# Optimization experiments

Measured on AMD Instinct MI355X. Metric: run time of the kernel, lower is better.

The kernel has to match this reference:

```python
import jax, jax.numpy as jnp
import numpy as np

N_SEND = 100000   # sender nodes
N_RECV = 100000   # receiver nodes
E = 600000        # edges
D = 128           # node feature channels (128x0e)
A = 8             # attr channels (8x0e)
S = 64            # edge scalar dim = fc_neurons[0]
H = 128           # fc hidden = fc_neurons[1]; tp.weight_numel = 128
NUM_NEIGHBORS = 32.0
SILU_NORM = 1.679177  # e3nn normalize2mom constant for silu: (E[silu(N(0,1))^2])^-0.5


def fctp(x, y, W):
    """e3nn FullyConnectedTensorProduct for all-scalar (0e) irreps:
    single 'uvw' path, path weight 1/sqrt(mul_u*mul_v)."""
    return jnp.einsum('nu,nv,uvw->nw', x, y, W) / np.sqrt(x.shape[1] * y.shape[1]).astype(np.float32)


def setup_inputs() -> dict:
    key = jax.random.key(0)
    ks = jax.random.split(key, 14)
    return {
        'sender_input': jax.random.normal(ks[0], (N_SEND, D), jnp.float32),
        'sender_attr': jax.random.normal(ks[1], (N_SEND, A), jnp.float32),
        'receiver_input': jax.random.normal(ks[2], (N_RECV, D), jnp.float32),
        'receiver_attr': jax.random.normal(ks[3], (N_RECV, A), jnp.float32),
        'edge_src': jax.random.randint(ks[4], (E,), 0, N_SEND, jnp.int32),
        'edge_dst': jax.random.randint(ks[5], (E,), 0, N_RECV, jnp.int32),
        'edge_attr': jax.random.normal(ks[6], (E, 1), jnp.float32),
        'edge_scalars': jax.random.normal(ks[7], (E, S), jnp.float32),
        # e3nn TP weights are initialized N(0,1)
        'W_sc': jax.random.normal(ks[8], (D, A, D), jnp.float32),
        'W_lin1': jax.random.normal(ks[9], (D, A, D), jnp.float32),
        'W_fc1': jax.random.normal(ks[10], (S, H), jnp.float32),
        'W_fc2': jax.random.normal(ks[11], (H, D), jnp.float32),
        'W_lin2': jax.random.normal(ks[12], (D, A, D), jnp.float32),
        'W_lin3': jax.random.normal(ks[13], (D, A, 1), jnp.float32),
    }


def reference(sender_input, sender_attr, receiver_input, receiver_attr,
              edge_src, edge_dst, edge_attr, edge_scalars,
              W_sc, W_lin1, W_fc1, W_fc2, W_lin2, W_lin3):
    # FullyConnectedNet([S, H, weight_numel], silu): act(x@W/sqrt(fan_in)), last layer linear
    h = SILU_NORM * jax.nn.silu(edge_scalars @ W_fc1 / np.sqrt(S).astype(np.float32))
    weight = h @ W_fc2 / np.sqrt(H).astype(np.float32)                     # [E, D] per-edge TP weights

    receiver_self_connection = fctp(receiver_input, receiver_attr, W_sc)   # [Nr, D]
    sender_features = fctp(sender_input, sender_attr, W_lin1)              # [Ns, D]

    # gather -> per-edge weighted ('uvu') tensor product with 1x0e edge_attr -> scatter-add
    edge_features = weight * sender_features[edge_src] * edge_attr         # [E, D]
    receiver_features = jax.ops.segment_sum(edge_features, edge_dst,
                                            num_segments=receiver_input.shape[0])
    receiver_features = receiver_features / np.sqrt(NUM_NEIGHBORS).astype(np.float32)

    receiver_conv_out = fctp(receiver_features, receiver_attr, W_lin2)     # [Nr, D]
    receiver_angle = 0.1 * fctp(receiver_features, receiver_attr, W_lin3)  # [Nr, 1]
    # sc.output_mask is all-ones for this irreps config, so sin gating applies to all channels
    return jnp.cos(receiver_angle) * receiver_self_connection + jnp.sin(receiver_angle) * receiver_conv_out
```

## Files before the change

### kernel.cpp

```cpp
#include <hip/hip_runtime.h>
#include <hip/hip_bf16.h>
#include <math.h>

#define NS 100000
#define NR 100000
#define NE 600000
#define SILU_NORM 1.679177f

typedef __attribute__((ext_vector_type(8))) short short8;
typedef __attribute__((ext_vector_type(4))) float f32x4;

static __device__ __forceinline__ short f2bf(float f) {
    return __builtin_bit_cast(short, __float2bfloat16(f));
}

#define GLDS16(g, l)                                                         \
    __builtin_amdgcn_global_load_lds(                                        \
        (const __attribute__((address_space(1))) unsigned int*)(const void*)(g), \
        (__attribute__((address_space(3))) unsigned int*)(void*)(l), 16, 0, 0)

__global__ void swz_kernel(const float* __restrict__ W,
                           __hip_bfloat16* __restrict__ out, int total)
{
    int idx = blockIdx.x * 256 + threadIdx.x;
    if (idx >= total) return;
    int s = idx >> 12, r = idx & 4095;
    int f = r >> 9;  r &= 511;
    int quad = r >> 7; r &= 127;
    int wl = r >> 3;
    int j = r & 7;
    int k = s * 32 + quad * 8 + j;
    int w = f * 16 + wl;
    out[idx] = __float2bfloat16(W[(size_t)k * 128 + w]);
}

__global__ __launch_bounds__(256) void fctp_mfma_kernel(
    const float* __restrict__ x, const float* __restrict__ y,
    const __hip_bfloat16* __restrict__ Wswz, float* __restrict__ out,
    float scale, int N)
{
    __shared__ __hip_bfloat16 Wb[8192];
    __shared__ float xs[128 * 8];

    const int tid = threadIdx.x;
    const int lane = tid & 63;
    const int wv = tid >> 6;
    const int quad = lane >> 4;
    const int wl = lane & 15;
    const int n0 = blockIdx.x * 128;

    float ya[2][8];
    #pragma unroll
    for (int mt = 0; mt < 2; ++mt) {
        int node = n0 + wv * 32 + mt * 16 + wl;
        if (node >= N) node = N - 1;
        const float4* yp = (const float4*)(y + (size_t)node * 8);
        float4 a = yp[0], b = yp[1];
        ya[mt][0] = a.x; ya[mt][1] = a.y; ya[mt][2] = a.z; ya[mt][3] = a.w;
        ya[mt][4] = b.x; ya[mt][5] = b.y; ya[mt][6] = b.z; ya[mt][7] = b.w;
    }

    f32x4 acc[2][8];
    #pragma unroll
    for (int mt = 0; mt < 2; ++mt)
        #pragma unroll
        for (int f = 0; f < 8; ++f)
            acc[mt][f] = (f32x4){0.f, 0.f, 0.f, 0.f};

    for (int cc = 0; cc < 16; ++cc) {
        __syncthreads();
        {
            const char* src = (const char*)(Wswz + (size_t)cc * 8192);
            #pragma unroll
            for (int i = 0; i < 4; ++i) {
                int off = (i * 256 + tid) * 16;
                GLDS16(src + off, (char*)Wb + off);
            }
            int nl = tid >> 1, c4 = (tid & 1) * 4;
            int node = n0 + nl;
            if (node >= N) node = N - 1;
            GLDS16(x + (size_t)node * 128 + cc * 8 + c4, (char*)xs + tid * 16);
        }
        __syncthreads();

        #pragma unroll
        for (int ks = 0; ks < 2; ++ks) {
            short8 bfr[8];
            #pragma unroll
            for (int f = 0; f < 8; ++f)
                bfr[f] = *(const short8*)((const short*)Wb +
                                          (size_t)ks * 4096 + (f * 64 + lane) * 8);
            #pragma unroll
            for (int mt = 0; mt < 2; ++mt) {
                float xv = xs[(wv * 32 + mt * 16 + wl) * 8 + ks * 4 + quad];
                short8 af;
                #pragma unroll
                for (int v = 0; v < 8; ++v) af[v] = f2bf(xv * ya[mt][v]);
                #pragma unroll
                for (int f = 0; f < 8; ++f)
                    acc[mt][f] = __builtin_amdgcn_mfma_f32_16x16x32_bf16(
                        af, bfr[f], acc[mt][f], 0, 0, 0);
            }
        }
    }

    #pragma unroll
    for (int mt = 0; mt < 2; ++mt) {
        #pragma unroll
        for (int r = 0; r < 4; ++r) {
            int node = n0 + wv * 32 + mt * 16 + quad * 4 + r;
            if (node < N) {
                #pragma unroll
                for (int f = 0; f < 8; ++f)
                    out[(size_t)node * 128 + f * 16 + wl] = acc[mt][f][r] * scale;
            }
        }
    }
}

__global__ __launch_bounds__(256) void edge_mfma_kernel(
    const int* __restrict__ esrc, const int* __restrict__ edst,
    const float* __restrict__ eattr, const float* __restrict__ escal,
    const __hip_bfloat16* __restrict__ W1swz,
    const __hip_bfloat16* __restrict__ W2swz,
    const float* __restrict__ sf, float* __restrict__ rfeat)
{
    __shared__ __hip_bfloat16 esA[8192];
    __shared__ __hip_bfloat16 Wb[16384];
    __shared__ __hip_bfloat16 hA[16384];

    const int tid = threadIdx.x;
    const int lane = tid & 63;
    const int wv = tid >> 6;
    const int quad = lane >> 4;
    const int wl = lane & 15;
    const int e0 = blockIdx.x * 128;

    #pragma unroll
    for (int i = 0; i < 4; ++i) {
        int c = i * 256 + tid;
        int l = c & 63, mtc = (c >> 6) & 7, s = c >> 9;
        int e = e0 + mtc * 16 + (l & 15);
        if (e >= NE) e = NE - 1;
        int kb = s * 32 + (l >> 4) * 8;
        const float4* p = (const float4*)(escal + (size_t)e * 64 + kb);
        float4 aa = p[0], bb = p[1];
        short8 v;
        v[0] = f2bf(aa.x); v[1] = f2bf(aa.y); v[2] = f2bf(aa.z); v[3] = f2bf(aa.w);
        v[4] = f2bf(bb.x); v[5] = f2bf(bb.y); v[6] = f2bf(bb.z); v[7] = f2bf(bb.w);
        *(short8*)((short*)esA + (size_t)c * 8) = v;
    }
    #pragma unroll
    for (int i = 0; i < 4; ++i) {
        int off = (i * 256 + tid) * 16;
        GLDS16((const char*)W1swz + off, (char*)Wb + off);
    }
    __syncthreads();

    f32x4 acc1[2][8];
    #pragma unroll
    for (int mt = 0; mt < 2; ++mt)
        #pragma unroll
        for (int f = 0; f < 8; ++f) acc1[mt][f] = (f32x4){0.f, 0.f, 0.f, 0.f};

    #pragma unroll
    for (int ks = 0; ks < 2; ++ks) {
        short8 bfr[8];
        #pragma unroll
        for (int f = 0; f < 8; ++f)
            bfr[f] = *(const short8*)((const short*)Wb +
                                      (size_t)ks * 4096 + (f * 64 + lane) * 8);
        #pragma unroll
        for (int mt = 0; mt < 2; ++mt) {
            int MT = wv * 2 + mt;
            short8 af = *(const short8*)((const short*)esA +
                                         ((size_t)(ks * 8 + MT) * 64 + lane) * 8);
            #pragma unroll
            for (int f = 0; f < 8; ++f)
                acc1[mt][f] = __builtin_amdgcn_mfma_f32_16x16x32_bf16(
                    af, bfr[f], acc1[mt][f], 0, 0, 0);
        }
    }

    #pragma unroll
    for (int mt = 0; mt < 2; ++mt) {
        int MT = wv * 2 + mt;
        #pragma unroll
        for (int f = 0; f < 8; ++f) {
            int s2 = f >> 1;
            int q2 = ((f & 1) * 2 + (wl >> 3)) & 3;
            int j2 = wl & 7;
            #pragma unroll
            for (int r = 0; r < 4; ++r) {
                float t = acc1[mt][f][r] * 0.125f;
                float h = SILU_NORM * t / (1.f + __expf(-t));
                int lpos = q2 * 16 + quad * 4 + r;
                ((short*)hA)[((size_t)(s2 * 8 + MT) * 64 + lpos) * 8 + j2] = f2bf(h);
            }
        }
    }
    __syncthreads();
    #pragma unroll
    for (int i = 0; i < 8; ++i) {
        int off = (i * 256 + tid) * 16;
        GLDS16((const char*)W2swz + off, (char*)Wb + off);
    }
    __syncthreads();

    f32x4 acc2[2][8];
    #pragma unroll
    for (int mt = 0; mt < 2; ++mt)
        #pragma unroll
        for (int f = 0; f < 8; ++f) acc2[mt][f] = (f32x4){0.f, 0.f, 0.f, 0.f};

    #pragma unroll
    for (int ks = 0; ks < 4; ++ks) {
        short8 bfr[8];
        #pragma unroll
        for (int f = 0; f < 8; ++f)
            bfr[f] = *(const short8*)((const short*)Wb +
                                      (size_t)ks * 4096 + (f * 64 + lane) * 8);
        #pragma unroll
        for (int mt = 0; mt < 2; ++mt) {
            int MT = wv * 2 + mt;
            short8 af = *(const short8*)((const short*)hA +
                                         ((size_t)(ks * 8 + MT) * 64 + lane) * 8);
            #pragma unroll
            for (int f = 0; f < 8; ++f)
                acc2[mt][f] = __builtin_amdgcn_mfma_f32_16x16x32_bf16(
                    af, bfr[f], acc2[mt][f], 0, 0, 0);
        }
    }

    const float s128 = 0.08838834764831845f;
    #pragma unroll
    for (int mt = 0; mt < 2; ++mt) {
        int MT = wv * 2 + mt;
        #pragma unroll
        for (int r = 0; r < 4; ++r) {
            int e = e0 + MT * 16 + quad * 4 + r;
            if (e < NE) {
                int src = esrc[e], dst = edst[e];
                float ea = eattr[e] * s128;
                #pragma unroll
                for (int f = 0; f < 8; ++f) {
                    float val = acc2[mt][f][r] * ea *
                                sf[(size_t)src * 128 + f * 16 + wl];
                    atomicAdd(&rfeat[(size_t)dst * 128 + f * 16 + wl], val);
                }
            }
        }
    }
}

__global__ __launch_bounds__(256) void angle_kernel(
    const float* __restrict__ rfeat, const float* __restrict__ rattr,
    const float* __restrict__ W3, float* __restrict__ angle)
{
    const int node = (int)((blockIdx.x * 256 + threadIdx.x) >> 6);
    const int lane = threadIdx.x & 63;
    float acc = 0.f;
    #pragma unroll
    for (int j = 0; j < 16; ++j) {
        int k = lane + 64 * j;
        int u = k >> 3, v = k & 7;
        acc += rfeat[(size_t)node * 128 + u] * rattr[(size_t)node * 8 + v] * W3[k];
    }
    #pragma unroll
    for (int off = 32; off; off >>= 1) acc += __shfl_down(acc, off);
    if (lane == 0) angle[node] = acc * 5.524271728019903e-4f;
}

__global__ __launch_bounds__(256) void combine_kernel(
    const float* __restrict__ conv, const float* __restrict__ rsc,
    const float* __restrict__ angle, float* __restrict__ out)
{
    int idx = blockIdx.x * 256 + threadIdx.x;
    float a = angle[idx >> 5];
    float ca = __cosf(a), sa = __sinf(a);
    float4 c = ((const float4*)conv)[idx];
    float4 s = ((const float4*)rsc)[idx];
    float4 o;
    o.x = ca * s.x + sa * c.x;
    o.y = ca * s.y + sa * c.y;
    o.z = ca * s.z + sa * c.z;
    o.w = ca * s.w + sa * c.w;
    ((float4*)out)[idx] = o;
}

extern "C" void kernel_launch(void* const* d_in, const int* in_sizes, int n_in,
                              void* d_out, int out_size, void* d_ws, size_t ws_size,
                              hipStream_t stream)
{
    const float* sender_input   = (const float*)d_in[0];
    const float* sender_attr    = (const float*)d_in[1];
    const float* receiver_input = (const float*)d_in[2];
    const float* receiver_attr  = (const float*)d_in[3];
    const int*   edge_src  = (const int*)d_in[4];
    const int*   edge_dst  = (const int*)d_in[5];
    const float* edge_attr = (const float*)d_in[6];
    const float* edge_scal = (const float*)d_in[7];
    const float* W_sc   = (const float*)d_in[8];
    const float* W_lin1 = (const float*)d_in[9];
    const float* W_fc1  = (const float*)d_in[10];
    const float* W_fc2  = (const float*)d_in[11];
    const float* W_lin2 = (const float*)d_in[12];
    const float* W_lin3 = (const float*)d_in[13];

    char* ws = (char*)d_ws;
    float* sf    = (float*)(ws);
    float* rfeat = (float*)(ws + 51200000);
    float* angle = (float*)(ws + 102400000);
    __hip_bfloat16* Wl1s = (__hip_bfloat16*)(ws + 102800000);
    __hip_bfloat16* Wscs = (__hip_bfloat16*)(ws + 103062144);
    __hip_bfloat16* Wl2s = (__hip_bfloat16*)(ws + 103324288);
    __hip_bfloat16* W1s  = (__hip_bfloat16*)(ws + 103586432);
    __hip_bfloat16* W2s  = (__hip_bfloat16*)(ws + 103602816);
    float* conv = sf;
    float* rsc  = rfeat;

    swz_kernel<<<512, 256, 0, stream>>>(W_lin1, Wl1s, 131072);
    swz_kernel<<<512, 256, 0, stream>>>(W_sc,   Wscs, 131072);
    swz_kernel<<<512, 256, 0, stream>>>(W_lin2, Wl2s, 131072);
    swz_kernel<<<32,  256, 0, stream>>>(W_fc1,  W1s,  8192);
    swz_kernel<<<64,  256, 0, stream>>>(W_fc2,  W2s,  16384);

    hipMemsetAsync(rfeat, 0, (size_t)NR * 128 * 4, stream);

    fctp_mfma_kernel<<<(NS + 127) / 128, 256, 0, stream>>>(
        sender_input, sender_attr, Wl1s, sf, 0.03125f, NS);
    edge_mfma_kernel<<<(NE + 127) / 128, 256, 0, stream>>>(
        edge_src, edge_dst, edge_attr, edge_scal, W1s, W2s, sf, rfeat);
    angle_kernel<<<NR / 4, 256, 0, stream>>>(rfeat, receiver_attr, W_lin3, angle);
    fctp_mfma_kernel<<<(NR + 127) / 128, 256, 0, stream>>>(
        rfeat, receiver_attr, Wl2s, conv, 0.005524271728019903f, NR);
    fctp_mfma_kernel<<<(NR + 127) / 128, 256, 0, stream>>>(
        receiver_input, receiver_attr, Wscs, rsc, 0.03125f, NR);
    combine_kernel<<<NR * 128 / 4 / 256, 256, 0, stream>>>(
        conv, rsc, angle, (float*)d_out);
}
```

Baseline: 817.8 us.

## Fuse lin2, angle and combine into one kernel; stream edge weights from global

Replaces the separate angle, lin2 FCTP and combine kernels with one conv_fuse_kernel. It computes the lin2 MFMA product, accumulates the lin3 angle from the same outer-product values, and writes the final cos/sin blend directly. This removes the conv and angle intermediate round-trips through global memory and two launches. The edge kernel also drops its LDS staging of W_fc1/W_fc2 and the scalar tile, reading the B fragments straight from global/L2 and A fragments into registers, with launch bounds set to 4 blocks. That cuts LDS use and barriers to raise occupancy, at the cost of repeated global weight loads per wave.

Result: faster. 747.7 us (-8.6%).

```diff
diff --git a/kernel.cpp b/kernel.cpp
--- a/kernel.cpp
+++ b/kernel.cpp
@@ -118,15 +118,13 @@
     }
 }
 
-__global__ __launch_bounds__(256) void edge_mfma_kernel(
+__global__ __launch_bounds__(256, 4) void edge_mfma_kernel(
     const int* __restrict__ esrc, const int* __restrict__ edst,
     const float* __restrict__ eattr, const float* __restrict__ escal,
     const __hip_bfloat16* __restrict__ W1swz,
     const __hip_bfloat16* __restrict__ W2swz,
     const float* __restrict__ sf, float* __restrict__ rfeat)
 {
-    __shared__ __hip_bfloat16 esA[8192];
-    __shared__ __hip_bfloat16 Wb[16384];
     __shared__ __hip_bfloat16 hA[16384];
 
     const int tid = threadIdx.x;
@@ -136,26 +134,20 @@
     const int wl = lane & 15;
     const int e0 = blockIdx.x * 128;
 
-    #pragma unroll
-    for (int i = 0; i < 4; ++i) {
-        int c = i * 256 + tid;
-        int l = c & 63, mtc = (c >> 6) & 7, s = c >> 9;
-        int e = e0 + mtc * 16 + (l & 15);
-        if (e >= NE) e = NE - 1;
-        int kb = s * 32 + (l >> 4) * 8;
-        const float4* p = (const float4*)(escal + (size_t)e * 64 + kb);
-        float4 aa = p[0], bb = p[1];
-        short8 v;
-        v[0] = f2bf(aa.x); v[1] = f2bf(aa.y); v[2] = f2bf(aa.z); v[3] = f2bf(aa.w);
-        v[4] = f2bf(bb.x); v[5] = f2bf(bb.y); v[6] = f2bf(bb.z); v[7] = f2bf(bb.w);
-        *(short8*)((short*)esA + (size_t)c * 8) = v;
-    }
-    #pragma unroll
-    for (int i = 0; i < 4; ++i) {
-        int off = (i * 256 + tid) * 16;
-        GLDS16((const char*)W1swz + off, (char*)Wb + off);
-    }
-    __syncthreads();
+    short8 af1[2][2];
+    #pragma unroll
+    for (int ks = 0; ks < 2; ++ks)
+        #pragma unroll
+        for (int mt = 0; mt < 2; ++mt) {
+            int e = e0 + (wv * 2 + mt) * 16 + wl;
+            if (e >= NE) e = NE - 1;
+            const float4* p = (const float4*)(escal + (size_t)e * 64 + ks * 32 + quad * 8);
+            float4 a = p[0], b = p[1];
+            short8 v;
+            v[0] = f2bf(a.x); v[1] = f2bf(a.y); v[2] = f2bf(a.z); v[3] = f2bf(a.w);
+            v[4] = f2bf(b.x); v[5] = f2bf(b.y); v[6] = f2bf(b.z); v[7] = f2bf(b.w);
+            af1[ks][mt] = v;
+        }
 
     f32x4 acc1[2][8];
     #pragma unroll
@@ -164,23 +156,16 @@
         for (int f = 0; f < 8; ++f) acc1[mt][f] = (f32x4){0.f, 0.f, 0.f, 0.f};
 
     #pragma unroll
-    for (int ks = 0; ks < 2; ++ks) {
-        short8 bfr[8];
-        #pragma unroll
-        for (int f = 0; f < 8; ++f)
-            bfr[f] = *(const short8*)((const short*)Wb +
-                                      (size_t)ks * 4096 + (f * 64 + lane) * 8);
-        #pragma unroll
-        for (int mt = 0; mt < 2; ++mt) {
-            int MT = wv * 2 + mt;
-            short8 af = *(const short8*)((const short*)esA +
-                                         ((size_t)(ks * 8 + MT) * 64 + lane) * 8);
-            #pragma unroll
-            for (int f = 0; f < 8; ++f)
-                acc1[mt][f] = __builtin_amdgcn_mfma_f32_16x16x32_bf16(
-                    af, bfr[f], acc1[mt][f], 0, 0, 0);
-        }
-    }
+    for (int ks = 0; ks < 2; ++ks)
+        #pragma unroll
+        for (int f = 0; f < 8; ++f) {
+            short8 bfr = *(const short8*)((const short*)W1swz +
+                                          (size_t)ks * 4096 + (f * 64 + lane) * 8);
+            acc1[0][f] = __builtin_amdgcn_mfma_f32_16x16x32_bf16(
+                af1[ks][0], bfr, acc1[0][f], 0, 0, 0);
+            acc1[1][f] = __builtin_amdgcn_mfma_f32_16x16x32_bf16(
+                af1[ks][1], bfr, acc1[1][f], 0, 0, 0);
+        }
 
     #pragma unroll
     for (int mt = 0; mt < 2; ++mt) {
@@ -200,12 +185,6 @@
         }
     }
     __syncthreads();
-    #pragma unroll
-    for (int i = 0; i < 8; ++i) {
-        int off = (i * 256 + tid) * 16;
-        GLDS16((const char*)W2swz + off, (char*)Wb + off);
-    }
-    __syncthreads();
 
     f32x4 acc2[2][8];
     #pragma unroll
@@ -215,20 +194,18 @@
 
     #pragma unroll
     for (int ks = 0; ks < 4; ++ks) {
-        short8 bfr[8];
-        #pragma unroll
-        for (int f = 0; f < 8; ++f)
-            bfr[f] = *(const short8*)((const short*)Wb +
-                                      (size_t)ks * 4096 + (f * 64 + lane) * 8);
-        #pragma unroll
-        for (int mt = 0; mt < 2; ++mt) {
-            int MT = wv * 2 + mt;
-            short8 af = *(const short8*)((const short*)hA +
-                                         ((size_t)(ks * 8 + MT) * 64 + lane) * 8);
-            #pragma unroll
-            for (int f = 0; f < 8; ++f)
-                acc2[mt][f] = __builtin_amdgcn_mfma_f32_16x16x32_bf16(
-                    af, bfr[f], acc2[mt][f], 0, 0, 0);
+        short8 afA = *(const short8*)((const short*)hA +
+                                      ((size_t)(ks * 8 + wv * 2 + 0) * 64 + lane) * 8);
+        short8 afB = *(const short8*)((const short*)hA +
+                                      ((size_t)(ks * 8 + wv * 2 + 1) * 64 + lane) * 8);
+        #pragma unroll
+        for (int f = 0; f < 8; ++f) {
+            short8 bfr = *(const short8*)((const short*)W2swz +
+                                          (size_t)ks * 4096 + (f * 64 + lane) * 8);
+            acc2[0][f] = __builtin_amdgcn_mfma_f32_16x16x32_bf16(
+                afA, bfr, acc2[0][f], 0, 0, 0);
+            acc2[1][f] = __builtin_amdgcn_mfma_f32_16x16x32_bf16(
+                afB, bfr, acc2[1][f], 0, 0, 0);
         }
     }
 
@@ -253,39 +230,110 @@
     }
 }
 
-__global__ __launch_bounds__(256) void angle_kernel(
-    const float* __restrict__ rfeat, const float* __restrict__ rattr,
-    const float* __restrict__ W3, float* __restrict__ angle)
-{
-    const int node = (int)((blockIdx.x * 256 + threadIdx.x) >> 6);
-    const int lane = threadIdx.x & 63;
-    float acc = 0.f;
-    #pragma unroll
-    for (int j = 0; j < 16; ++j) {
-        int k = lane + 64 * j;
-        int u = k >> 3, v = k & 7;
-        acc += rfeat[(size_t)node * 128 + u] * rattr[(size_t)node * 8 + v] * W3[k];
-    }
-    #pragma unroll
-    for (int off = 32; off; off >>= 1) acc += __shfl_down(acc, off);
-    if (lane == 0) angle[node] = acc * 5.524271728019903e-4f;
-}
-
-__global__ __launch_bounds__(256) void combine_kernel(
-    const float* __restrict__ conv, const float* __restrict__ rsc,
-    const float* __restrict__ angle, float* __restrict__ out)
-{
-    int idx = blockIdx.x * 256 + threadIdx.x;
-    float a = angle[idx >> 5];
-    float ca = __cosf(a), sa = __sinf(a);
-    float4 c = ((const float4*)conv)[idx];
-    float4 s = ((const float4*)rsc)[idx];
-    float4 o;
-    o.x = ca * s.x + sa * c.x;
-    o.y = ca * s.y + sa * c.y;
-    o.z = ca * s.z + sa * c.z;
-    o.w = ca * s.w + sa * c.w;
-    ((float4*)out)[idx] = o;
+__global__ __launch_bounds__(256) void conv_fuse_kernel(
+    const float* __restrict__ x, const float* __restrict__ y,
+    const __hip_bfloat16* __restrict__ Wswz, const float* __restrict__ W3,
+    const float* __restrict__ rsc, float* __restrict__ out, int N)
+{
+    __shared__ __hip_bfloat16 Wb[8192];
+    __shared__ float xs[128 * 8];
+
+    const int tid = threadIdx.x;
+    const int lane = tid & 63;
+    const int wv = tid >> 6;
+    const int quad = lane >> 4;
+    const int wl = lane & 15;
+    const int n0 = blockIdx.x * 128;
+
+    float ya[2][8];
+    #pragma unroll
+    for (int mt = 0; mt < 2; ++mt) {
+        int node = n0 + wv * 32 + mt * 16 + wl;
+        if (node >= N) node = N - 1;
+        const float4* yp = (const float4*)(y + (size_t)node * 8);
+        float4 a = yp[0], b = yp[1];
+        ya[mt][0] = a.x; ya[mt][1] = a.y; ya[mt][2] = a.z; ya[mt][3] = a.w;
+        ya[mt][4] = b.x; ya[mt][5] = b.y; ya[mt][6] = b.z; ya[mt][7] = b.w;
+    }
+
+    f32x4 acc[2][8];
+    #pragma unroll
+    for (int mt = 0; mt < 2; ++mt)
+        #pragma unroll
+        for (int f = 0; f < 8; ++f)
+            acc[mt][f] = (f32x4){0.f, 0.f, 0.f, 0.f};
+    float aacc[2] = {0.f, 0.f};
+
+    for (int cc = 0; cc < 16; ++cc) {
+        __syncthreads();
+        {
+            const char* src = (const char*)(Wswz + (size_t)cc * 8192);
+            #pragma unroll
+            for (int i = 0; i < 4; ++i) {
+                int off = (i * 256 + tid) * 16;
+                GLDS16(src + off, (char*)Wb + off);
+            }
+            int nl = tid >> 1, c4 = (tid & 1) * 4;
+            int node = n0 + nl;
+            if (node >= N) node = N - 1;
+            GLDS16(x + (size_t)node * 128 + cc * 8 + c4, (char*)xs + tid * 16);
+        }
+        __syncthreads();
+
+        #pragma unroll
+        for (int ks = 0; ks < 2; ++ks) {
+            short8 bfr[8];
+            #pragma unroll
+            for (int f = 0; f < 8; ++f)
+                bfr[f] = *(const short8*)((const short*)Wb +
+                                          (size_t)ks * 4096 + (f * 64 + lane) * 8);
+            const float4* wp = (const float4*)(W3 + ((cc * 8 + ks * 4 + quad) * 8));
+            float4 w3a = wp[0], w3b = wp[1];
+            float w3v[8] = {w3a.x, w3a.y, w3a.z, w3a.w, w3b.x, w3b.y, w3b.z, w3b.w};
+            #pragma unroll
+            for (int mt = 0; mt < 2; ++mt) {
+                float xv = xs[(wv * 32 + mt * 16 + wl) * 8 + ks * 4 + quad];
+                short8 af;
+                #pragma unroll
+                for (int v = 0; v < 8; ++v) {
+                    float p = xv * ya[mt][v];
+                    af[v] = f2bf(p);
+                    aacc[mt] += p * w3v[v];
+                }
+                #pragma unroll
+                for (int f = 0; f < 8; ++f)
+                    acc[mt][f] = __builtin_amdgcn_mfma_f32_16x16x32_bf16(
+                        af, bfr[f], acc[mt][f], 0, 0, 0);
+            }
+        }
+    }
+
+    float ared[2];
+    #pragma unroll
+    for (int mt = 0; mt < 2; ++mt) {
+        float a = aacc[mt];
+        a += __shfl_xor(a, 16);
+        a += __shfl_xor(a, 32);
+        ared[mt] = a * 5.524271728019903e-4f;
+    }
+
+    const float cs = 5.524271728019903e-3f;
+    #pragma unroll
+    for (int mt = 0; mt < 2; ++mt) {
+        #pragma unroll
+        for (int r = 0; r < 4; ++r) {
+            int node = n0 + wv * 32 + mt * 16 + quad * 4 + r;
+            float a = __shfl(ared[mt], quad * 4 + r);
+            if (node < N) {
+                float ca = __cosf(a), sa = __sinf(a);
+                #pragma unroll
+                for (int f = 0; f < 8; ++f) {
+                    size_t o = (size_t)node * 128 + f * 16 + wl;
+                    out[o] = ca * rsc[o] + sa * (acc[mt][f][r] * cs);
+                }
+            }
+        }
+    }
 }
 
 extern "C" void kernel_launch(void* const* d_in, const int* in_sizes, int n_in,
@@ -310,14 +358,12 @@
     char* ws = (char*)d_ws;
     float* sf    = (float*)(ws);
     float* rfeat = (float*)(ws + 51200000);
-    float* angle = (float*)(ws + 102400000);
-    __hip_bfloat16* Wl1s = (__hip_bfloat16*)(ws + 102800000);
-    __hip_bfloat16* Wscs = (__hip_bfloat16*)(ws + 103062144);
-    __hip_bfloat16* Wl2s = (__hip_bfloat16*)(ws + 103324288);
-    __hip_bfloat16* W1s  = (__hip_bfloat16*)(ws + 103586432);
-    __hip_bfloat16* W2s  = (__hip_bfloat16*)(ws + 103602816);
-    float* conv = sf;
-    float* rsc  = rfeat;
+    __hip_bfloat16* Wl1s = (__hip_bfloat16*)(ws + 102400000);
+    __hip_bfloat16* Wscs = (__hip_bfloat16*)(ws + 102662144);
+    __hip_bfloat16* Wl2s = (__hip_bfloat16*)(ws + 102924288);
+    __hip_bfloat16* W1s  = (__hip_bfloat16*)(ws + 103186432);
+    __hip_bfloat16* W2s  = (__hip_bfloat16*)(ws + 103202816);
+    float* rsc = sf;
 
     swz_kernel<<<512, 256, 0, stream>>>(W_lin1, Wl1s, 131072);
     swz_kernel<<<512, 256, 0, stream>>>(W_sc,   Wscs, 131072);
@@ -331,11 +377,8 @@
         sender_input, sender_attr, Wl1s, sf, 0.03125f, NS);
     edge_mfma_kernel<<<(NE + 127) / 128, 256, 0, stream>>>(
         edge_src, edge_dst, edge_attr, edge_scal, W1s, W2s, sf, rfeat);
-    angle_kernel<<<NR / 4, 256, 0, stream>>>(rfeat, receiver_attr, W_lin3, angle);
-    fctp_mfma_kernel<<<(NR + 127) / 128, 256, 0, stream>>>(
-        rfeat, receiver_attr, Wl2s, conv, 0.005524271728019903f, NR);
     fctp_mfma_kernel<<<(NR + 127) / 128, 256, 0, stream>>>(
         receiver_input, receiver_attr, Wscs, rsc, 0.03125f, NR);
-    combine_kernel<<<NR * 128 / 4 / 256, 256, 0, stream>>>(
-        conv, rsc, angle, (float*)d_out);
-}
+    conv_fuse_kernel<<<(NR + 127) / 128, 256, 0, stream>>>(
+        rfeat, receiver_attr, Wl2s, W_lin3, rsc, (float*)d_out, NR);
+}
```
